# Kernel optimization log

Measured on AMD Instinct MI355X. Metric: run time of the kernel, lower is better.

## Reference

```python
import jax, jax.numpy as jnp
import numpy as np

EPS = 1e-8
THR = 1e-6


def setup_inputs() -> dict:
    key = jax.random.key(0)
    ks = jax.random.split(key, 16)
    B, N, E, F, H, NH = 2, 8192, 131072, 128, 256, 4
    D = H // NH          # per-head width = 64
    FEAT = 2 * F + 12    # 268 = 2F + radial + dist + dot + 9 so3
    s = 0.05
    return {
        "h": jax.random.normal(ks[0], (B, N, F), jnp.float32),
        "coord": jax.random.normal(ks[1], (B, N, 3), jnp.float32),
        "edge_index": jax.random.randint(ks[2], (2, E), 0, N),
        "edge_w1": jax.random.normal(ks[3], (NH, FEAT, D), jnp.float32) * s,
        "edge_b1": jnp.zeros((NH, D), jnp.float32),
        "edge_w2": jax.random.normal(ks[4], (NH, D, D), jnp.float32) * s,
        "edge_b2": jnp.zeros((NH, D), jnp.float32),
        "ln_g": jnp.ones((H,), jnp.float32),
        "ln_b": jnp.zeros((H,), jnp.float32),
        "node_w1": jax.random.normal(ks[5], (H + F, H), jnp.float32) * s,
        "node_b1": jnp.zeros((H,), jnp.float32),
        "node_w2": jax.random.normal(ks[6], (H, F), jnp.float32) * s,
        "node_b2": jnp.zeros((F,), jnp.float32),
        "coord_w1": jax.random.normal(ks[7], (H, H), jnp.float32) * s,
        "coord_b1": jnp.zeros((H,), jnp.float32),
        "coord_w2": jax.random.normal(ks[8], (H, 1), jnp.float32) * 0.001,  # xavier gain 0.001
    }


def reference(h, coord, edge_index, edge_w1, edge_b1, edge_w2, edge_b2,
              ln_g, ln_b, node_w1, node_b1, node_w2, node_b2,
              coord_w1, coord_b1, coord_w2):
    B, N, F = h.shape
    row, col = edge_index[0], edge_index[1]
    ci, ck = coord[:, row], coord[:, col]            # (B,E,3) gathers
    coord_diff = ci - ck
    radial = jnp.sum(coord_diff * coord_diff, axis=-1, keepdims=True)
    dist = jnp.sqrt(radial)
    dot = jnp.sum(ci * ck, axis=-1, keepdims=True)
    # SO3 local frame per edge
    a = coord_diff / (dist + EPS)
    cr = jnp.cross(ci, ck)
    b = cr / (jnp.linalg.norm(cr, axis=-1, keepdims=True) + EPS)
    c = jnp.cross(a, b)
    bad = ((jnp.linalg.norm(a, axis=-1) < THR) |
           (jnp.linalg.norm(b, axis=-1) < THR) |
           (jnp.linalg.norm(c, axis=-1) < THR))
    so3 = jnp.stack([a, b, c], axis=-1)              # (B,E,3,3) columns a,b,c
    eye = jnp.broadcast_to(jnp.eye(3, dtype=so3.dtype), so3.shape)
    so3 = jnp.where(bad[..., None, None], eye, so3).reshape(B, -1, 9)
    # edge features -> multi-head edge MLPs
    feat = jnp.concatenate([h[:, row], h[:, col], radial, dist, dot, so3], axis=-1)  # (B,E,268)
    hmid = jax.nn.silu(jnp.einsum('bef,hfd->bhed', feat, edge_w1) + edge_b1[None, :, None, :])
    heads = jnp.einsum('bhed,hdk->bhek', hmid, edge_w2) + edge_b2[None, :, None, :]
    combined = jnp.moveaxis(heads, 1, 2).reshape(B, heads.shape[2], -1)  # (B,E,H)
    mu = jnp.mean(combined, axis=-1, keepdims=True)
    var = jnp.var(combined, axis=-1, keepdims=True)
    edge_feat = (combined - mu) / jnp.sqrt(var + 1e-5) * ln_g + ln_b
    # coordinate update: scatter-add weighted coord_diff
    w = jax.nn.silu(edge_feat @ coord_w1 + coord_b1) @ coord_w2   # (B,E,1)
    seg = lambda d: jax.ops.segment_sum(d, row, num_segments=N)
    coord_out = coord + jax.vmap(seg)(coord_diff * w)
    # node update: scatter-add edge features then MLP with residual
    agg = jax.vmap(seg)(edge_feat)                                # (B,N,H)
    out = jnp.concatenate([h, agg], axis=-1)
    out = jax.nn.silu(out @ node_w1 + node_b1) @ node_w2 + node_b2
    return h + out, coord_out
```

## Files before the change

### kernel.cpp

```cpp
#include <hip/hip_runtime.h>
#include <cstdint>
#include <cstddef>

#define BB 2
#define NN 8192
#define EE 131072
#define FFdim 128
#define HHdim 256
#define NHEAD 4
#define DHEAD 64
#define FEATD 268
#define K1PAD 288
#define SF 296
#define SH 264
#define TE 64
#define NT 32
#define SA 392
#define SM 264

typedef short bf16x8 __attribute__((ext_vector_type(8)));
typedef float floatx4 __attribute__((ext_vector_type(4)));

__device__ __forceinline__ float silu_f(float x) {
    return x * __fdividef(1.0f, 1.0f + __expf(-x));
}
__device__ __forceinline__ unsigned short f2bf(float x) {
    unsigned int u = __float_as_uint(x);
    unsigned int r = (u + 0x7fffu + ((u >> 16) & 1u)) >> 16;
    return (unsigned short)r;
}
__device__ __forceinline__ float bf2f(unsigned short u) {
    return __uint_as_float(((unsigned int)u) << 16);
}
__device__ __forceinline__ int operm(int p) { return ((p & 3) << 4) | (p >> 2); }

#define W1T_ELEMS (256 * K1PAD)
#define W2T_ELEMS (256 * 64)
#define CW1T_ELEMS (256 * 256)
#define NW1T_ELEMS (256 * 384)
#define NW2T_ELEMS (128 * 256)
#define WT_A (W1T_ELEMS)
#define WT_B (W1T_ELEMS + W2T_ELEMS)
#define WT_C (W1T_ELEMS + W2T_ELEMS + CW1T_ELEMS)
#define WT_D (WT_C + NW1T_ELEMS)
#define WT_E (WT_D + NW2T_ELEMS)
__global__ void prep_weights(const float* __restrict__ w1,
                             const float* __restrict__ w2,
                             const float* __restrict__ cw1,
                             const float* __restrict__ nw1,
                             const float* __restrict__ nw2,
                             unsigned short* __restrict__ w1T,
                             unsigned short* __restrict__ w2T,
                             unsigned short* __restrict__ cw1T,
                             unsigned short* __restrict__ nw1T,
                             unsigned short* __restrict__ nw2T,
                             int* __restrict__ counts) {
    int idx = blockIdx.x * blockDim.x + threadIdx.x;
    if (idx < WT_A) {
        int n = idx / K1PAD, k = idx % K1PAD;
        int hh = n >> 6, d = n & 63;
        float v = (k < FEATD) ? w1[((size_t)hh * FEATD + k) * DHEAD + d] : 0.f;
        w1T[idx] = f2bf(v);
    } else if (idx < WT_B) {
        int j = idx - WT_A;
        int n = j >> 6, p = j & 63;
        int hh = n >> 6, dout = n & 63;
        int din = operm(p);
        w2T[j] = f2bf(w2[(size_t)hh * 4096 + din * 64 + dout]);
    } else if (idx < WT_C) {
        int j = idx - WT_B;
        int n = j >> 8, P = j & 255;
        int ko = (P >> 6) * 64 + operm(P & 63);
        cw1T[j] = f2bf(cw1[ko * 256 + n]);
    } else if (idx < WT_D) {
        int j = idx - WT_C;
        int n = j / 384, k = j % 384;
        int ko = (k < 128) ? k : 128 + ((k - 128) >> 6) * 64 + operm(k & 63);
        nw1T[j] = f2bf(nw1[ko * 256 + n]);
    } else if (idx < WT_E) {
        int j = idx - WT_D;
        int n = j >> 8, P = j & 255;
        int ko = (P >> 6) * 64 + operm(P & 63);
        nw2T[j] = f2bf(nw2[ko * 128 + n]);
    } else if (idx < WT_E + NN) {
        counts[idx - WT_E] = 0;
    }
}

__global__ void csr_count(const int* __restrict__ eidx, int* __restrict__ counts) {
    int e = blockIdx.x * 256 + threadIdx.x;
    atomicAdd(&counts[eidx[e]], 1);
}

__global__ void csr_scan(const int* __restrict__ counts,
                         int* __restrict__ offsets,
                         int* __restrict__ cursor) {
    __shared__ int wsum[4];
    const int t = threadIdx.x;
    const int base = t * 32;
    int local[32];
    int s = 0;
#pragma unroll
    for (int i = 0; i < 32; ++i) { local[i] = counts[base + i]; s += local[i]; }
    const int lane = t & 63, w = t >> 6;
    int v = s;
#pragma unroll
    for (int off = 1; off < 64; off <<= 1) {
        int u = __shfl_up(v, off, 64);
        if (lane >= off) v += u;
    }
    if (lane == 63) wsum[w] = v;
    __syncthreads();
    int wbase = 0;
    for (int i = 0; i < w; ++i) wbase += wsum[i];
    int run = wbase + v - s;
#pragma unroll
    for (int i = 0; i < 32; ++i) {
        offsets[base + i] = run;
        cursor[base + i] = run;
        run += local[i];
    }
    if (t == 255) offsets[NN] = run;
}

__global__ void csr_fill(const int* __restrict__ eidx,
                         int* __restrict__ cursor, int* __restrict__ perm) {
    int e = blockIdx.x * 256 + threadIdx.x;
    int r = eidx[e];
    int pos = atomicAdd(&cursor[r], 1);
    perm[e] = pos;
}

__global__ __launch_bounds__(256, 3)
void edge_kernel(const float* __restrict__ h,
                 const float* __restrict__ coord,
                 const int* __restrict__ eidx,
                 const int* __restrict__ perm,
                 const unsigned short* __restrict__ w1T, const float* __restrict__ b1,
                 const unsigned short* __restrict__ w2T, const float* __restrict__ b2,
                 const float* __restrict__ lng, const float* __restrict__ lnb,
                 const unsigned short* __restrict__ cw1T, const float* __restrict__ cb1,
                 const float* __restrict__ cw2,
                 unsigned short* __restrict__ efb, float4* __restrict__ wd) {
    __shared__ unsigned short bufA[TE * SF];
    __shared__ int slot_s[TE];
    __shared__ float cd_s[TE][3];
    __shared__ float2 lnred[TE][4];
    __shared__ float mu_s[TE], rs_s[TE];
    __shared__ float wpart[TE][4];

    const int tid = threadIdx.x;
    const int b = blockIdx.y;
    const int e0 = blockIdx.x * TE;
    const int lane = tid & 63;
    const int w = tid >> 6;
    const int lm = lane & 15;
    const int quad = lane >> 4;
    const int koff = quad * 8;

    if (tid < TE) {
        const int e = e0 + tid;
        const int r = eidx[e], c = eidx[EE + e];
        slot_s[tid] = perm[e];
        const float* pi = coord + ((size_t)b * NN + r) * 3;
        const float* pk = coord + ((size_t)b * NN + c) * 3;
        float ci0 = pi[0], ci1 = pi[1], ci2 = pi[2];
        float ck0 = pk[0], ck1 = pk[1], ck2 = pk[2];
        float dx = ci0 - ck0, dy = ci1 - ck1, dz = ci2 - ck2;
        float radial = dx * dx + dy * dy + dz * dz;
        float dist = sqrtf(radial);
        float dotv = ci0 * ck0 + ci1 * ck1 + ci2 * ck2;
        float inva = __fdividef(1.0f, dist + 1e-8f);
        float a0 = dx * inva, a1 = dy * inva, a2 = dz * inva;
        float cr0 = ci1 * ck2 - ci2 * ck1;
        float cr1 = ci2 * ck0 - ci0 * ck2;
        float cr2 = ci0 * ck1 - ci1 * ck0;
        float nb = sqrtf(cr0 * cr0 + cr1 * cr1 + cr2 * cr2);
        float invb = __fdividef(1.0f, nb + 1e-8f);
        float b0 = cr0 * invb, b1v = cr1 * invb, b2v = cr2 * invb;
        float c0 = a1 * b2v - a2 * b1v;
        float c1 = a2 * b0 - a0 * b2v;
        float c2 = a0 * b1v - a1 * b0;
        float na = sqrtf(a0 * a0 + a1 * a1 + a2 * a2);
        float nbn = sqrtf(b0 * b0 + b1v * b1v + b2v * b2v);
        float nc = sqrtf(c0 * c0 + c1 * c1 + c2 * c2);
        bool bad = (na < 1e-6f) || (nbn < 1e-6f) || (nc < 1e-6f);
        float s[12];
        s[0] = radial; s[1] = dist; s[2] = dotv;
        if (bad) {
            s[3] = 1.f; s[4] = 0.f; s[5] = 0.f;
            s[6] = 0.f; s[7] = 1.f; s[8] = 0.f;
            s[9] = 0.f; s[10] = 0.f; s[11] = 1.f;
        } else {
            s[3] = a0;  s[4] = b0;  s[5] = c0;
            s[6] = a1;  s[7] = b1v; s[8] = c1;
            s[9] = a2;  s[10] = b2v; s[11] = c2;
        }
        unsigned short* fp = &bufA[tid * SF];
#pragma unroll
        for (int q = 0; q < 12; ++q) fp[256 + q] = f2bf(s[q]);
#pragma unroll
        for (int q = FEATD; q < K1PAD; ++q) fp[q] = 0;
        cd_s[tid][0] = dx; cd_s[tid][1] = dy; cd_s[tid][2] = dz;
    }
    for (int idx = tid; idx < TE * 64; idx += 256) {
        const int e = idx >> 6, c4 = idx & 63;
        const int node = (c4 < 32) ? eidx[e0 + e] : eidx[EE + e0 + e];
        const int cc = (c4 < 32) ? c4 * 4 : (c4 - 32) * 4;
        float4 v = *(const float4*)&h[((size_t)b * NN + node) * FFdim + cc];
        ushort4 u;
        u.x = f2bf(v.x); u.y = f2bf(v.y); u.z = f2bf(v.z); u.w = f2bf(v.w);
        *(ushort4*)&bufA[e * SF + c4 * 4] = u;
    }
    __syncthreads();

    floatx4 acc[4][4];
#pragma unroll
    for (int i = 0; i < 4; ++i)
#pragma unroll
        for (int j = 0; j < 4; ++j)
#pragma unroll
            for (int q = 0; q < 4; ++q) acc[i][j][q] = 0.f;
#pragma unroll
    for (int ks = 0; ks < K1PAD / 32; ++ks) {
        const int kb = ks * 32 + koff;
        bf16x8 a[4], bfr[4];
#pragma unroll
        for (int rt = 0; rt < 4; ++rt)
            a[rt] = *(const bf16x8*)&bufA[(rt * 16 + lm) * SF + kb];
#pragma unroll
        for (int ct = 0; ct < 4; ++ct)
            bfr[ct] = *(const bf16x8*)&w1T[(size_t)(w * 64 + ct * 16 + lm) * K1PAD + kb];
#pragma unroll
        for (int rt = 0; rt < 4; ++rt)
#pragma unroll
            for (int ct = 0; ct < 4; ++ct)
                acc[rt][ct] = __builtin_amdgcn_mfma_f32_16x16x32_bf16(
                    a[rt], bfr[ct], acc[rt][ct], 0, 0, 0);
    }
    float bias1[4];
#pragma unroll
    for (int ct = 0; ct < 4; ++ct) bias1[ct] = b1[w * 64 + ct * 16 + lm];
    __syncthreads();
#pragma unroll
    for (int rt = 0; rt < 4; ++rt)
#pragma unroll
        for (int reg = 0; reg < 4; ++reg) {
            const int row = rt * 16 + quad * 4 + reg;
            ushort4 pk;
            pk.x = f2bf(silu_f(acc[rt][0][reg] + bias1[0]));
            pk.y = f2bf(silu_f(acc[rt][1][reg] + bias1[1]));
            pk.z = f2bf(silu_f(acc[rt][2][reg] + bias1[2]));
            pk.w = f2bf(silu_f(acc[rt][3][reg] + bias1[3]));
            *(ushort4*)&bufA[row * SH + w * 64 + lm * 4] = pk;
        }

    floatx4 acc2[4][4];
#pragma unroll
    for (int i = 0; i < 4; ++i)
#pragma unroll
        for (int j = 0; j < 4; ++j)
#pragma unroll
            for (int q = 0; q < 4; ++q) acc2[i][j][q] = 0.f;
#pragma unroll
    for (int ks = 0; ks < 2; ++ks) {
        const int kb = ks * 32 + koff;
        bf16x8 a[4], bfr[4];
#pragma unroll
        for (int rt = 0; rt < 4; ++rt)
            a[rt] = *(const bf16x8*)&bufA[(rt * 16 + lm) * SH + w * 64 + kb];
#pragma unroll
        for (int ct = 0; ct < 4; ++ct)
            bfr[ct] = *(const bf16x8*)&w2T[(size_t)(w * 64 + ct * 16 + lm) * 64 + kb];
#pragma unroll
        for (int rt = 0; rt < 4; ++rt)
#pragma unroll
            for (int ct = 0; ct < 4; ++ct)
                acc2[rt][ct] = __builtin_amdgcn_mfma_f32_16x16x32_bf16(
                    a[rt], bfr[ct], acc2[rt][ct], 0, 0, 0);
    }
    float bias2[4];
#pragma unroll
    for (int ct = 0; ct < 4; ++ct) bias2[ct] = b2[w * 64 + ct * 16 + lm];
#pragma unroll
    for (int rt = 0; rt < 4; ++rt)
#pragma unroll
        for (int reg = 0; reg < 4; ++reg) {
            float s = 0.f, s2 = 0.f;
#pragma unroll
            for (int ct = 0; ct < 4; ++ct) {
                float v = acc2[rt][ct][reg] + bias2[ct];
                acc2[rt][ct][reg] = v;
                s += v; s2 += v * v;
            }
#pragma unroll
            for (int m = 1; m <= 8; m <<= 1) {
                s += __shfl_xor(s, m, 64);
                s2 += __shfl_xor(s2, m, 64);
            }
            if (lm == 0) {
                const int row = rt * 16 + quad * 4 + reg;
                lnred[row][w] = make_float2(s, s2);
            }
        }
    __syncthreads();
    if (tid < TE) {
        float s = 0.f, s2 = 0.f;
#pragma unroll
        for (int ww = 0; ww < 4; ++ww) { s += lnred[tid][ww].x; s2 += lnred[tid][ww].y; }
        float mean = s * (1.0f / 256.0f);
        float var = s2 * (1.0f / 256.0f) - mean * mean;
        mu_s[tid] = mean;
        rs_s[tid] = rsqrtf(var + 1e-5f);
    }
    __syncthreads();
    {
        float gv[4], bv[4];
#pragma unroll
        for (int ct = 0; ct < 4; ++ct) {
            const int col = w * 64 + ct * 16 + lm;
            gv[ct] = lng[col]; bv[ct] = lnb[col];
        }
#pragma unroll
        for (int rt = 0; rt < 4; ++rt)
#pragma unroll
            for (int reg = 0; reg < 4; ++reg) {
                const int row = rt * 16 + quad * 4 + reg;
                const float mu = mu_s[row], rs = rs_s[row];
                ushort4 pk;
                pk.x = f2bf((acc2[rt][0][reg] - mu) * rs * gv[0] + bv[0]);
                pk.y = f2bf((acc2[rt][1][reg] - mu) * rs * gv[1] + bv[1]);
                pk.z = f2bf((acc2[rt][2][reg] - mu) * rs * gv[2] + bv[2]);
                pk.w = f2bf((acc2[rt][3][reg] - mu) * rs * gv[3] + bv[3]);
                *(ushort4*)&bufA[row * SH + w * 64 + lm * 4] = pk;
            }
    }
    __syncthreads();

    floatx4 acc3[4][4];
#pragma unroll
    for (int i = 0; i < 4; ++i)
#pragma unroll
        for (int j = 0; j < 4; ++j)
#pragma unroll
            for (int q = 0; q < 4; ++q) acc3[i][j][q] = 0.f;
#pragma unroll
    for (int ks = 0; ks < 8; ++ks) {
        const int kb = ks * 32 + koff;
        bf16x8 a[4], bfr[4];
#pragma unroll
        for (int rt = 0; rt < 4; ++rt)
            a[rt] = *(const bf16x8*)&bufA[(rt * 16 + lm) * SH + kb];
#pragma unroll
        for (int ct = 0; ct < 4; ++ct)
            bfr[ct] = *(const bf16x8*)&cw1T[(size_t)(w * 64 + ct * 16 + lm) * 256 + kb];
#pragma unroll
        for (int rt = 0; rt < 4; ++rt)
#pragma unroll
            for (int ct = 0; ct < 4; ++ct)
                acc3[rt][ct] = __builtin_amdgcn_mfma_f32_16x16x32_bf16(
                    a[rt], bfr[ct], acc3[rt][ct], 0, 0, 0);
    }
    {
        float cb[4], cwv[4];
#pragma unroll
        for (int ct = 0; ct < 4; ++ct) {
            const int col = w * 64 + ct * 16 + lm;
            cb[ct] = cb1[col]; cwv[ct] = cw2[col];
        }
#pragma unroll
        for (int rt = 0; rt < 4; ++rt)
#pragma unroll
            for (int reg = 0; reg < 4; ++reg) {
                float s = 0.f;
#pragma unroll
                for (int ct = 0; ct < 4; ++ct)
                    s += silu_f(acc3[rt][ct][reg] + cb[ct]) * cwv[ct];
#pragma unroll
                for (int m = 1; m <= 8; m <<= 1) s += __shfl_xor(s, m, 64);
                if (lm == 0) wpart[rt * 16 + quad * 4 + reg][w] = s;
            }
    }
    __syncthreads();

    if (tid < TE) {
        float ww = wpart[tid][0] + wpart[tid][1] + wpart[tid][2] + wpart[tid][3];
        float4 o = { cd_s[tid][0] * ww, cd_s[tid][1] * ww, cd_s[tid][2] * ww, 0.f };
        wd[(size_t)b * EE + slot_s[tid]] = o;
    }
    for (int idx = tid; idx < TE * 32; idx += 256) {
        const int e = idx >> 5, c = idx & 31;
        uint4 v = *(const uint4*)&bufA[e * SH + c * 8];
        *(uint4*)&efb[((size_t)b * EE + slot_s[e]) * HHdim + c * 8] = v;
    }
}

__global__ __launch_bounds__(256, 4)
void node_kernel(const float* __restrict__ h,
                 const float* __restrict__ coord,
                 const unsigned short* __restrict__ efb,
                 const float4* __restrict__ wd,
                 const int* __restrict__ offsets,
                 const unsigned short* __restrict__ nw1T, const float* __restrict__ nb1,
                 const unsigned short* __restrict__ nw2T, const float* __restrict__ nb2,
                 float* __restrict__ hout, float* __restrict__ coord_out) {
    __shared__ unsigned short bufN[NT * SA];

    const int tid = threadIdx.x;
    const int b = blockIdx.y;
    const int n0 = blockIdx.x * NT;
    const int lane = tid & 63;
    const int w = tid >> 6;
    const int lm = lane & 15;
    const int quad = lane >> 4;
    const int koff = quad * 8;

    for (int idx = tid; idx < NT * 32; idx += 256) {
        const int r = idx >> 5, c4 = idx & 31;
        float4 v = *(const float4*)&h[((size_t)b * NN + n0 + r) * FFdim + c4 * 4];
        ushort4 u;
        u.x = f2bf(v.x); u.y = f2bf(v.y); u.z = f2bf(v.z); u.w = f2bf(v.w);
        *(ushort4*)&bufN[r * SA + c4 * 4] = u;
    }

    for (int i = 0; i < 8; ++i) {
        const int r = w * 8 + i;
        const int n = n0 + r;
        const int o0 = offsets[n], o1 = offsets[n + 1];
        float a0 = 0.f, a1 = 0.f, a2 = 0.f, a3 = 0.f;
        const unsigned short* ebase = efb + (size_t)b * EE * HHdim + lane * 4;
        int j = o0;
        for (; j + 4 <= o1; j += 4) {
            ushort4 u0 = *(const ushort4*)(ebase + (size_t)(j + 0) * HHdim);
            ushort4 u1 = *(const ushort4*)(ebase + (size_t)(j + 1) * HHdim);
            ushort4 u2 = *(const ushort4*)(ebase + (size_t)(j + 2) * HHdim);
            ushort4 u3 = *(const ushort4*)(ebase + (size_t)(j + 3) * HHdim);
            a0 += bf2f(u0.x) + bf2f(u1.x) + bf2f(u2.x) + bf2f(u3.x);
            a1 += bf2f(u0.y) + bf2f(u1.y) + bf2f(u2.y) + bf2f(u3.y);
            a2 += bf2f(u0.z) + bf2f(u1.z) + bf2f(u2.z) + bf2f(u3.z);
            a3 += bf2f(u0.w) + bf2f(u1.w) + bf2f(u2.w) + bf2f(u3.w);
        }
        for (; j < o1; ++j) {
            ushort4 u = *(const ushort4*)(ebase + (size_t)j * HHdim);
            a0 += bf2f(u.x); a1 += bf2f(u.y); a2 += bf2f(u.z); a3 += bf2f(u.w);
        }
        ushort4 o;
        o.x = f2bf(a0); o.y = f2bf(a1); o.z = f2bf(a2); o.w = f2bf(a3);
        *(ushort4*)&bufN[r * SA + FFdim + lane * 4] = o;

        float sx = 0.f, sy = 0.f, sz = 0.f;
        for (int jj = o0 + lane; jj < o1; jj += 64) {
            float4 t = wd[(size_t)b * EE + jj];
            sx += t.x; sy += t.y; sz += t.z;
        }
#pragma unroll
        for (int m = 1; m < 64; m <<= 1) {
            sx += __shfl_xor(sx, m, 64);
            sy += __shfl_xor(sy, m, 64);
            sz += __shfl_xor(sz, m, 64);
        }
        if (lane < 3) {
            const size_t cb = ((size_t)b * NN + n) * 3 + lane;
            float s = (lane == 0) ? sx : (lane == 1) ? sy : sz;
            coord_out[cb] = coord[cb] + s;
        }
    }
    __syncthreads();

    floatx4 acc[2][4];
#pragma unroll
    for (int i = 0; i < 2; ++i)
#pragma unroll
        for (int j = 0; j < 4; ++j)
#pragma unroll
            for (int q = 0; q < 4; ++q) acc[i][j][q] = 0.f;
#pragma unroll
    for (int ks = 0; ks < 12; ++ks) {
        const int kb = ks * 32 + koff;
        bf16x8 a[2], bfr[4];
#pragma unroll
        for (int rt = 0; rt < 2; ++rt)
            a[rt] = *(const bf16x8*)&bufN[(rt * 16 + lm) * SA + kb];
#pragma unroll
        for (int ct = 0; ct < 4; ++ct)
            bfr[ct] = *(const bf16x8*)&nw1T[(size_t)(w * 64 + ct * 16 + lm) * 384 + kb];
#pragma unroll
        for (int rt = 0; rt < 2; ++rt)
#pragma unroll
            for (int ct = 0; ct < 4; ++ct)
                acc[rt][ct] = __builtin_amdgcn_mfma_f32_16x16x32_bf16(
                    a[rt], bfr[ct], acc[rt][ct], 0, 0, 0);
    }
    float nb1v[4];
#pragma unroll
    for (int ct = 0; ct < 4; ++ct) nb1v[ct] = nb1[w * 64 + ct * 16 + lm];
    __syncthreads();
#pragma unroll
    for (int rt = 0; rt < 2; ++rt)
#pragma unroll
        for (int reg = 0; reg < 4; ++reg) {
            const int row = rt * 16 + quad * 4 + reg;
            ushort4 pk;
            pk.x = f2bf(silu_f(acc[rt][0][reg] + nb1v[0]));
            pk.y = f2bf(silu_f(acc[rt][1][reg] + nb1v[1]));
            pk.z = f2bf(silu_f(acc[rt][2][reg] + nb1v[2]));
            pk.w = f2bf(silu_f(acc[rt][3][reg] + nb1v[3]));
            *(ushort4*)&bufN[row * SM + w * 64 + lm * 4] = pk;
        }
    __syncthreads();

    floatx4 accb[2][2];
#pragma unroll
    for (int i = 0; i < 2; ++i)
#pragma unroll
        for (int j = 0; j < 2; ++j)
#pragma unroll
            for (int q = 0; q < 4; ++q) accb[i][j][q] = 0.f;
#pragma unroll
    for (int ks = 0; ks < 8; ++ks) {
        const int kb = ks * 32 + koff;
        bf16x8 a[2], bfr[2];
#pragma unroll
        for (int rt = 0; rt < 2; ++rt)
            a[rt] = *(const bf16x8*)&bufN[(rt * 16 + lm) * SM + kb];
#pragma unroll
        for (int ct = 0; ct < 2; ++ct)
            bfr[ct] = *(const bf16x8*)&nw2T[(size_t)(w * 32 + ct * 16 + lm) * 256 + kb];
#pragma unroll
        for (int rt = 0; rt < 2; ++rt)
#pragma unroll
            for (int ct = 0; ct < 2; ++ct)
                accb[rt][ct] = __builtin_amdgcn_mfma_f32_16x16x32_bf16(
                    a[rt], bfr[ct], accb[rt][ct], 0, 0, 0);
    }
#pragma unroll
    for (int ct = 0; ct < 2; ++ct) {
        const int col = w * 32 + ct * 16 + lm;
        const float bias = nb2[col];
#pragma unroll
        for (int rt = 0; rt < 2; ++rt)
#pragma unroll
            for (int reg = 0; reg < 4; ++reg) {
                const int row = rt * 16 + quad * 4 + reg;
                const size_t gi = ((size_t)b * NN + n0 + row) * FFdim + col;
                hout[gi] = accb[rt][ct][reg] + bias + h[gi];
            }
    }
}

extern "C" void kernel_launch(void* const* d_in, const int* in_sizes, int n_in,
                              void* d_out, int out_size, void* d_ws, size_t ws_size,
                              hipStream_t stream) {
    const float* h     = (const float*)d_in[0];
    const float* coord = (const float*)d_in[1];
    const int*   eidx  = (const int*)d_in[2];
    const float* w1    = (const float*)d_in[3];
    const float* b1    = (const float*)d_in[4];
    const float* w2    = (const float*)d_in[5];
    const float* b2    = (const float*)d_in[6];
    const float* lng   = (const float*)d_in[7];
    const float* lnb   = (const float*)d_in[8];
    const float* nw1   = (const float*)d_in[9];
    const float* nb1   = (const float*)d_in[10];
    const float* nw2   = (const float*)d_in[11];
    const float* nb2   = (const float*)d_in[12];
    const float* cw1   = (const float*)d_in[13];
    const float* cb1   = (const float*)d_in[14];
    const float* cw2   = (const float*)d_in[15];

    float* hout = (float*)d_out;
    float* coord_out = hout + (size_t)BB * NN * FFdim;

    char* p = (char*)d_ws;
    float4* wd = (float4*)p;                   p += (size_t)BB * EE * 16;
    unsigned short* efb = (unsigned short*)p;  p += (size_t)BB * EE * HHdim * 2;
    unsigned short* w1T = (unsigned short*)p;  p += (size_t)W1T_ELEMS * 2;
    unsigned short* w2T = (unsigned short*)p;  p += (size_t)W2T_ELEMS * 2;
    unsigned short* cw1T = (unsigned short*)p; p += (size_t)CW1T_ELEMS * 2;
    unsigned short* nw1T = (unsigned short*)p; p += (size_t)NW1T_ELEMS * 2;
    unsigned short* nw2T = (unsigned short*)p; p += (size_t)NW2T_ELEMS * 2;
    int* counts = (int*)p;                     p += (size_t)NN * 4;
    int* offsets = (int*)p;                    p += (size_t)(NN + 1) * 4;
    int* cursor = (int*)p;                     p += (size_t)NN * 4;
    int* perm = (int*)p;                       p += (size_t)EE * 4;

    hipLaunchKernelGGL(prep_weights, dim3((WT_E + NN) / 256), dim3(256),
                       0, stream, w1, w2, cw1, nw1, nw2,
                       w1T, w2T, cw1T, nw1T, nw2T, counts);
    hipLaunchKernelGGL(csr_count, dim3(EE / 256), dim3(256), 0, stream, eidx, counts);
    hipLaunchKernelGGL(csr_scan, dim3(1), dim3(256), 0, stream, counts, offsets, cursor);
    hipLaunchKernelGGL(csr_fill, dim3(EE / 256), dim3(256), 0, stream, eidx, cursor, perm);
    hipLaunchKernelGGL(edge_kernel, dim3(EE / TE, BB), dim3(256), 0, stream,
                       h, coord, eidx, perm, w1T, b1, w2T, b2, lng, lnb, cw1T, cb1, cw2,
                       efb, wd);
    hipLaunchKernelGGL(node_kernel, dim3(NN / NT, BB), dim3(256), 0, stream,
                       h, coord, efb, wd, offsets, nw1T, nb1, nw2T, nb2,
                       hout, coord_out);
}
```

Measured before the change: 362.8 us.

## Pre-convert h to bf16 once and shrink edge kernel shared memory for occupancy

Adds a bf16 copy of h built in the prep kernel, so the edge and node kernels gather 16-byte bf16 vectors instead of fp32 rows that each block converts itself. The LayerNorm partial sums now go through shared-memory atomics, and the reduction scratch arrays are merged into one buffer. Launch bounds for the edge kernel rise from 3 to 4 blocks per CU. The aim is to halve the random-gather traffic and raise occupancy, at the cost of an extra 4 MB conversion pass, shared atomics, and possible register spills under the tighter bound.

```diff
diff --git a/kernel.cpp b/kernel.cpp
--- a/kernel.cpp
+++ b/kernel.cpp
@@ -39,21 +39,26 @@
 #define CW1T_ELEMS (256 * 256)
 #define NW1T_ELEMS (256 * 384)
 #define NW2T_ELEMS (128 * 256)
+#define HBF_ELEMS (BB * NN * FFdim)
 #define WT_A (W1T_ELEMS)
 #define WT_B (W1T_ELEMS + W2T_ELEMS)
 #define WT_C (W1T_ELEMS + W2T_ELEMS + CW1T_ELEMS)
 #define WT_D (WT_C + NW1T_ELEMS)
 #define WT_E (WT_D + NW2T_ELEMS)
+#define WT_F (WT_E + NN)
+#define WT_G (WT_F + HBF_ELEMS)
 __global__ void prep_weights(const float* __restrict__ w1,
                              const float* __restrict__ w2,
                              const float* __restrict__ cw1,
                              const float* __restrict__ nw1,
                              const float* __restrict__ nw2,
+                             const float* __restrict__ h,
                              unsigned short* __restrict__ w1T,
                              unsigned short* __restrict__ w2T,
                              unsigned short* __restrict__ cw1T,
                              unsigned short* __restrict__ nw1T,
                              unsigned short* __restrict__ nw2T,
+                             unsigned short* __restrict__ hbf,
                              int* __restrict__ counts) {
     int idx = blockIdx.x * blockDim.x + threadIdx.x;
     if (idx < WT_A) {
@@ -82,8 +87,11 @@
         int n = j >> 8, P = j & 255;
         int ko = (P >> 6) * 64 + operm(P & 63);
         nw2T[j] = f2bf(nw2[ko * 128 + n]);
-    } else if (idx < WT_E + NN) {
+    } else if (idx < WT_F) {
         counts[idx - WT_E] = 0;
+    } else if (idx < WT_G) {
+        int j = idx - WT_F;
+        hbf[j] = f2bf(h[j]);
     }
 }
 
@@ -131,8 +139,8 @@
     perm[e] = pos;
 }
 
-__global__ __launch_bounds__(256, 3)
-void edge_kernel(const float* __restrict__ h,
+__global__ __launch_bounds__(256, 4)
+void edge_kernel(const unsigned short* __restrict__ hbf,
                  const float* __restrict__ coord,
                  const int* __restrict__ eidx,
                  const int* __restrict__ perm,
@@ -145,9 +153,8 @@
     __shared__ unsigned short bufA[TE * SF];
     __shared__ int slot_s[TE];
     __shared__ float cd_s[TE][3];
-    __shared__ float2 lnred[TE][4];
-    __shared__ float mu_s[TE], rs_s[TE];
-    __shared__ float wpart[TE][4];
+    __shared__ float lns[TE], lns2[TE];
+    __shared__ float scr[TE * 4];
 
     const int tid = threadIdx.x;
     const int b = blockIdx.y;
@@ -159,6 +166,7 @@
     const int koff = quad * 8;
 
     if (tid < TE) {
+        lns[tid] = 0.f; lns2[tid] = 0.f;
         const int e = e0 + tid;
         const int r = eidx[e], c = eidx[EE + e];
         slot_s[tid] = perm[e];
@@ -203,14 +211,12 @@
         for (int q = FEATD; q < K1PAD; ++q) fp[q] = 0;
         cd_s[tid][0] = dx; cd_s[tid][1] = dy; cd_s[tid][2] = dz;
     }
-    for (int idx = tid; idx < TE * 64; idx += 256) {
-        const int e = idx >> 6, c4 = idx & 63;
-        const int node = (c4 < 32) ? eidx[e0 + e] : eidx[EE + e0 + e];
-        const int cc = (c4 < 32) ? c4 * 4 : (c4 - 32) * 4;
-        float4 v = *(const float4*)&h[((size_t)b * NN + node) * FFdim + cc];
-        ushort4 u;
-        u.x = f2bf(v.x); u.y = f2bf(v.y); u.z = f2bf(v.z); u.w = f2bf(v.w);
-        *(ushort4*)&bufA[e * SF + c4 * 4] = u;
+    for (int idx = tid; idx < TE * 32; idx += 256) {
+        const int e = idx >> 5, c16 = idx & 31;
+        const int node = (c16 < 16) ? eidx[e0 + e] : eidx[EE + e0 + e];
+        const int cc = (c16 & 15) * 8;
+        uint4 v = *(const uint4*)&hbf[((size_t)b * NN + node) * FFdim + cc];
+        *(uint4*)&bufA[e * SF + c16 * 8] = v;
     }
     __syncthreads();
 
@@ -300,18 +306,16 @@
             }
             if (lm == 0) {
                 const int row = rt * 16 + quad * 4 + reg;
-                lnred[row][w] = make_float2(s, s2);
+                atomicAdd(&lns[row], s);
+                atomicAdd(&lns2[row], s2);
             }
         }
     __syncthreads();
     if (tid < TE) {
-        float s = 0.f, s2 = 0.f;
-#pragma unroll
-        for (int ww = 0; ww < 4; ++ww) { s += lnred[tid][ww].x; s2 += lnred[tid][ww].y; }
-        float mean = s * (1.0f / 256.0f);
-        float var = s2 * (1.0f / 256.0f) - mean * mean;
-        mu_s[tid] = mean;
-        rs_s[tid] = rsqrtf(var + 1e-5f);
+        float mean = lns[tid] * (1.0f / 256.0f);
+        float var = lns2[tid] * (1.0f / 256.0f) - mean * mean;
+        scr[tid] = mean;
+        scr[TE + tid] = rsqrtf(var + 1e-5f);
     }
     __syncthreads();
     {
@@ -326,7 +330,7 @@
 #pragma unroll
             for (int reg = 0; reg < 4; ++reg) {
                 const int row = rt * 16 + quad * 4 + reg;
-                const float mu = mu_s[row], rs = rs_s[row];
+                const float mu = scr[row], rs = scr[TE + row];
                 ushort4 pk;
                 pk.x = f2bf((acc2[rt][0][reg] - mu) * rs * gv[0] + bv[0]);
                 pk.y = f2bf((acc2[rt][1][reg] - mu) * rs * gv[1] + bv[1]);
@@ -378,13 +382,13 @@
                     s += silu_f(acc3[rt][ct][reg] + cb[ct]) * cwv[ct];
 #pragma unroll
                 for (int m = 1; m <= 8; m <<= 1) s += __shfl_xor(s, m, 64);
-                if (lm == 0) wpart[rt * 16 + quad * 4 + reg][w] = s;
+                if (lm == 0) scr[(rt * 16 + quad * 4 + reg) * 4 + w] = s;
             }
     }
     __syncthreads();
 
     if (tid < TE) {
-        float ww = wpart[tid][0] + wpart[tid][1] + wpart[tid][2] + wpart[tid][3];
+        float ww = scr[tid * 4] + scr[tid * 4 + 1] + scr[tid * 4 + 2] + scr[tid * 4 + 3];
         float4 o = { cd_s[tid][0] * ww, cd_s[tid][1] * ww, cd_s[tid][2] * ww, 0.f };
         wd[(size_t)b * EE + slot_s[tid]] = o;
     }
@@ -397,6 +401,7 @@
 
 __global__ __launch_bounds__(256, 4)
 void node_kernel(const float* __restrict__ h,
+                 const unsigned short* __restrict__ hbf,
                  const float* __restrict__ coord,
                  const unsigned short* __restrict__ efb,
                  const float4* __restrict__ wd,
@@ -415,12 +420,10 @@
     const int quad = lane >> 4;
     const int koff = quad * 8;
 
-    for (int idx = tid; idx < NT * 32; idx += 256) {
-        const int r = idx >> 5, c4 = idx & 31;
-        float4 v = *(const float4*)&h[((size_t)b * NN + n0 + r) * FFdim + c4 * 4];
-        ushort4 u;
-        u.x = f2bf(v.x); u.y = f2bf(v.y); u.z = f2bf(v.z); u.w = f2bf(v.w);
-        *(ushort4*)&bufN[r * SA + c4 * 4] = u;
+    for (int idx = tid; idx < NT * 16; idx += 256) {
+        const int r = idx >> 4, c8 = idx & 15;
+        uint4 v = *(const uint4*)&hbf[((size_t)b * NN + n0 + r) * FFdim + c8 * 8];
+        *(uint4*)&bufN[r * SA + c8 * 8] = v;
     }
 
     for (int i = 0; i < 8; ++i) {
@@ -574,6 +577,7 @@
     char* p = (char*)d_ws;
     float4* wd = (float4*)p;                   p += (size_t)BB * EE * 16;
     unsigned short* efb = (unsigned short*)p;  p += (size_t)BB * EE * HHdim * 2;
+    unsigned short* hbf = (unsigned short*)p;  p += (size_t)HBF_ELEMS * 2;
     unsigned short* w1T = (unsigned short*)p;  p += (size_t)W1T_ELEMS * 2;
     unsigned short* w2T = (unsigned short*)p;  p += (size_t)W2T_ELEMS * 2;
     unsigned short* cw1T = (unsigned short*)p; p += (size_t)CW1T_ELEMS * 2;
@@ -584,16 +588,16 @@
     int* cursor = (int*)p;                     p += (size_t)NN * 4;
     int* perm = (int*)p;                       p += (size_t)EE * 4;
 
-    hipLaunchKernelGGL(prep_weights, dim3((WT_E + NN) / 256), dim3(256),
-                       0, stream, w1, w2, cw1, nw1, nw2,
-                       w1T, w2T, cw1T, nw1T, nw2T, counts);
+    hipLaunchKernelGGL(prep_weights, dim3((WT_G + 255) / 256), dim3(256),
+                       0, stream, w1, w2, cw1, nw1, nw2, h,
+                       w1T, w2T, cw1T, nw1T, nw2T, hbf, counts);
     hipLaunchKernelGGL(csr_count, dim3(EE / 256), dim3(256), 0, stream, eidx, counts);
     hipLaunchKernelGGL(csr_scan, dim3(1), dim3(256), 0, stream, counts, offsets, cursor);
     hipLaunchKernelGGL(csr_fill, dim3(EE / 256), dim3(256), 0, stream, eidx, cursor, perm);
     hipLaunchKernelGGL(edge_kernel, dim3(EE / TE, BB), dim3(256), 0, stream,
-                       h, coord, eidx, perm, w1T, b1, w2T, b2, lng, lnb, cw1T, cb1, cw2,
+                       hbf, coord, eidx, perm, w1T, b1, w2T, b2, lng, lnb, cw1T, cb1, cw2,
                        efb, wd);
     hipLaunchKernelGGL(node_kernel, dim3(NN / NT, BB), dim3(256), 0, stream,
-                       h, coord, efb, wd, offsets, nw1T, nb1, nw2T, nb2,
+                       h, hbf, coord, efb, wd, offsets, nw1T, nb1, nw2T, nb2,
                        hout, coord_out);
 }
```

Result: faster. 345.8 us (-4.7%).
